# Kernel tuning notes

Measured on AMD Instinct MI355X. Metric: run time of the kernel, lower is better.

## Reference

```python
import jax, jax.numpy as jnp
import numpy as np

LN_EPS = 1e-5


def conv2d(x, w, b, stride, pad):
    # x: NCHW, w: OIHW
    y = jax.lax.conv_general_dilated(
        x, w, (stride, stride), [(pad, pad), (pad, pad)],
        dimension_numbers=("NCHW", "OIHW", "NCHW"))
    return y + b[None, :, None, None]


def gdn(x, gamma, beta):
    # y_c = x_c / sqrt(beta_c + sum_j gamma_cj * x_j^2)  (1x1 conv on x^2)
    norm = jnp.einsum("bchw,dc->bdhw", x * x, gamma) + beta[None, :, None, None]
    return x / jnp.sqrt(norm)


def layernorm(x, w, b):
    mu = jnp.mean(x, axis=-1, keepdims=True)
    var = jnp.var(x, axis=-1, keepdims=True)
    return (x - mu) / jnp.sqrt(var + LN_EPS) * w + b


def setup_inputs() -> dict:
    key = jax.random.key(0)
    ks = jax.random.split(key, 16)
    r = lambda i, shape: (jax.random.normal(ks[i], shape) * 0.02).astype(jnp.float32)
    N, M, K, D = 128, 192, 192, 128
    return {
        "x_p": jax.random.normal(ks[0], (4, 16, 3, 64, 64), jnp.float32),
        "y_g": jax.random.normal(ks[1], (64, K, 32), jnp.float32),
        "conv1_w": r(2, (N, 3, 5, 5)), "conv1_b": jnp.zeros((N,), jnp.float32),
        "gamma1": (0.1 * jnp.eye(N) + 1e-3).astype(jnp.float32), "beta1": jnp.ones((N,), jnp.float32),
        "conv2_w": r(3, (N, N, 5, 5)), "conv2_b": jnp.zeros((N,), jnp.float32),
        "gamma2": (0.1 * jnp.eye(N) + 1e-3).astype(jnp.float32), "beta2": jnp.ones((N,), jnp.float32),
        "conv3_w": r(4, (M, N, 3, 3)), "conv3_b": jnp.zeros((M,), jnp.float32),
        "ln_q_w": jnp.ones((M,), jnp.float32), "ln_q_b": jnp.zeros((M,), jnp.float32),
        "ln_kv_w": jnp.ones((K,), jnp.float32), "ln_kv_b": jnp.zeros((K,), jnp.float32),
        "ln_out_w": jnp.ones((M,), jnp.float32), "ln_out_b": jnp.zeros((M,), jnp.float32),
        "Wq": r(5, (D, M)), "Wk": r(6, (D, K)), "v_w": r(7, (1, D)),
        "Wv": r(8, (M, K)), "out_w": r(9, (M, M)), "out_b": jnp.zeros((M,), jnp.float32),
    }


def reference(x_p, y_g, conv1_w, conv1_b, gamma1, beta1, conv2_w, conv2_b,
              gamma2, beta2, conv3_w, conv3_b, ln_q_w, ln_q_b, ln_kv_w, ln_kv_b,
              ln_out_w, ln_out_b, Wq, Wk, v_w, Wv, out_w, out_b):
    B, P, C, Hp, Wp = x_p.shape
    x = x_p.reshape(B * P, C, Hp, Wp)
    # local encoder: conv s2 -> GDN -> conv s2 -> GDN -> conv s1 k3
    x = gdn(conv2d(x, conv1_w, conv1_b, 2, 2), gamma1, beta1)
    x = gdn(conv2d(x, conv2_w, conv2_b, 2, 2), gamma2, beta2)
    y_local = conv2d(x, conv3_w, conv3_b, 1, 1)          # (BP, M, h, w)
    BP, M, h, w = y_local.shape
    q = y_local.reshape(BP, M, h * w).transpose(0, 2, 1)  # (BP, Tq, M)
    kv = y_g.reshape(BP, y_g.shape[1], -1).transpose(0, 2, 1)  # (BP, Tk, K)
    q = layernorm(q, ln_q_w, ln_q_b)
    kv = layernorm(kv, ln_kv_w, ln_kv_b)
    # Bahdanau additive attention
    q_proj = jnp.einsum("bqm,dm->bqd", q, Wq)            # (BP, Tq, D)
    k_proj = jnp.einsum("bkc,dc->bkd", kv, Wk)           # (BP, Tk, D)
    energy = jnp.einsum("bqkd,d->bqk",
                        jnp.tanh(q_proj[:, :, None, :] + k_proj[:, None, :, :]),
                        v_w[0])                           # (BP, Tq, Tk)
    alpha = jax.nn.softmax(energy, axis=-1)
    v_proj = jnp.einsum("bkc,mc->bkm", kv, Wv)           # (BP, Tk, M)
    context = jnp.einsum("bqk,bkm->bqm", alpha, v_proj)
    context = jnp.einsum("bqm,nm->bqn", context, out_w) + out_b
    fused = layernorm(q + context, ln_out_w, ln_out_b)
    return fused.transpose(0, 2, 1).reshape(BP, M, h, w)
```

## Files before the change

kernel.cpp:

```cpp
#include <hip/hip_runtime.h>
#include <cstddef>
#include <cstdint>


typedef __bf16 bf16x8 __attribute__((ext_vector_type(8)));
typedef float floatx4 __attribute__((ext_vector_type(4)));
typedef unsigned short ushortT;
typedef unsigned short ushort8v __attribute__((ext_vector_type(8)));

#if __has_builtin(__builtin_amdgcn_exp2f)
#define EXP2F(x) __builtin_amdgcn_exp2f(x)
#else
#define EXP2F(x) exp2f(x)
#endif
#if __has_builtin(__builtin_amdgcn_rcpf)
#define RCPF(x) __builtin_amdgcn_rcpf(x)
#else
#define RCPF(x) (1.f / (x))
#endif

__device__ __forceinline__ ushortT f2bf(float f) {
  unsigned u = __builtin_bit_cast(unsigned, f);
  unsigned r = (u + 0x7FFFu + ((u >> 16) & 1u)) >> 16;
  return (ushortT)r;
}
__device__ __forceinline__ float bf2f(ushortT u) {
  return __builtin_bit_cast(float, ((unsigned)u) << 16);
}

static constexpr size_t OFF_X2BF = 4194304;
static constexpr size_t OFF_X3BF = 9437184;
static constexpr size_t OFF_QRAW = 10485760;
static constexpr size_t OFF_WBQ  = 21299200;
static constexpr size_t OFF_WBK  = 21311488;
static constexpr size_t OFF_WBV  = 21323776;
static constexpr size_t OFF_WBO  = 21342208;
static constexpr size_t OFF_WT2  = 26079232;
static constexpr size_t OFF_WT3  = 26284032;
static constexpr size_t OFF_WC1  = 26394624;
static constexpr size_t OFF_GB1  = 26406912;
static constexpr size_t OFF_GB2  = 26415104;
static constexpr size_t OFF_KP   = 0;
static constexpr size_t OFF_VT   = 262144;

__device__ __constant__ int d_TWI2[4][9] = {{ 0, 2, 4,10,12,14,20,22,24},
                                            { 1, 3,11,13,21,23, 0, 0, 0},
                                            { 5, 7, 9,15,17,19, 0, 0, 0},
                                            { 6, 8,16,18, 0, 0, 0, 0, 0}};
__device__ __constant__ int d_NT2[4] = {9, 6, 6, 4};

__device__ void dev_convw3(const float* w, ushortT* wt, int mode, int total,
                           int idx) {
  if (idx >= total) return;
  int j    = idx & 7;
  int om   = (idx >> 3) & 63;
  int kg   = (idx >> 9) & 3;
  int slab = idx >> 11;
  int mt, s, tap, T;
  if (mode == 0) {
    int ph;
    if (slab < 72) ph = 0; else if (slab < 120) ph = 1;
    else if (slab < 168) ph = 2; else ph = 3;
    const int st[4] = {0, 72, 120, 168};
    const int ns[4] = {36, 24, 24, 16};
    int rel = slab - st[ph];
    mt = rel / ns[ph]; s = rel % ns[ph];
    tap = d_TWI2[ph][s >> 2]; T = 25;
  } else {
    mt = slab / 36; s = slab % 36; tap = s >> 2; T = 9;
  }
  int cc = s & 3;
  int c  = cc * 32 + kg * 8 + j;
  int oc = mt * 64 + om;
  wt[idx] = f2bf(w[(size_t)(oc * 128 + c) * T + tap]);
}

__device__ void dev_convw1(const float* w, ushortT* wt, int idx) {
  if (idx >= 20480) return;
  int k    = idx & 31;
  int oc   = (idx >> 5) & 127;
  int slab = idx >> 12;
  int ph, i;
  if (slab < 2) { ph = 0; i = slab; } else { ph = slab - 1; i = 0; }
  int kg = k >> 3, jj = k & 7;
  int tidx = i * 8 + jj;
  float val = 0.f;
  if (kg < 3 && tidx < d_NT2[ph]) {
    int tap = d_TWI2[ph][tidx];
    val = w[(size_t)(oc * 3 + kg) * 25 + tap];
  }
  wt[idx] = f2bf(val);
}

__device__ void dev_wcast(const float* w, ushortT* wb, int total, float scale,
                          int idx) {
  if (idx < total) wb[idx] = f2bf(w[idx] * scale);
}

__global__ __launch_bounds__(256) void prep_kernel(
    const float* __restrict__ conv2_w, ushortT* __restrict__ wt2,
    const float* __restrict__ conv3_w, ushortT* __restrict__ wt3,
    const float* __restrict__ conv1_w, ushortT* __restrict__ wc1,
    const float* __restrict__ Wq, ushortT* __restrict__ wbq,
    const float* __restrict__ Wk, ushortT* __restrict__ wbk,
    const float* __restrict__ Wv, ushortT* __restrict__ wbv,
    const float* __restrict__ out_w, ushortT* __restrict__ wbo,
    const float* __restrict__ gamma1, ushortT* __restrict__ gb1,
    const float* __restrict__ gamma2, ushortT* __restrict__ gb2) {
  constexpr float C2LE = 2.88539008177792681f;
  int blk = blockIdx.x, tid = threadIdx.x;
  if (blk < 1600)      dev_convw3(conv2_w, wt2, 0, 409600, blk * 256 + tid);
  else if (blk < 2464) dev_convw3(conv3_w, wt3, 1, 221184, (blk - 1600) * 256 + tid);
  else if (blk < 2544) dev_convw1(conv1_w, wc1, (blk - 2464) * 256 + tid);
  else if (blk < 2640) dev_wcast(Wq, wbq, 24576, C2LE, (blk - 2544) * 256 + tid);
  else if (blk < 2736) dev_wcast(Wk, wbk, 24576, C2LE, (blk - 2640) * 256 + tid);
  else if (blk < 2880) dev_wcast(Wv, wbv, 36864, 1.f, (blk - 2736) * 256 + tid);
  else if (blk < 3024) dev_wcast(out_w, wbo, 36864, 1.f, (blk - 2880) * 256 + tid);
  else if (blk < 3088) dev_wcast(gamma1, gb1, 16384, 1.f, (blk - 3024) * 256 + tid);
  else                 dev_wcast(gamma2, gb2, 16384, 1.f, (blk - 3088) * 256 + tid);
}

__global__ __launch_bounds__(256, 2) void conv1_gdn_kernel(
    const float* __restrict__ x, const ushortT* __restrict__ wc1,
    const float* __restrict__ bias, const ushortT* __restrict__ gb1,
    const float* __restrict__ beta1, ushortT* __restrict__ outb) {
  int b  = blockIdx.x >> 3;
  int yg = blockIdx.x & 7;
  int y0 = yg * 4;

  int wave = threadIdx.x >> 6;
  int lane = threadIdx.x & 63;
  int ln15 = lane & 15;
  int kg   = lane >> 4;
  int tid  = threadIdx.x;

  __shared__ ushortT smem[28416];
  ushortT* simg = smem;
  ushortT* sA   = smem + 2816;

  for (int j = tid; j < 1408; j += 256) ((unsigned*)simg)[j] = 0u;
  __syncthreads();

  int ihBase = 2 * y0 - 2;
  const float* xb = x + (size_t)b * 3 * 4096;
  for (int j = tid; j < 576; j += 256) {
    int q = j & 15;
    int rr = j >> 4;
    int c = rr / 12, ihl = rr % 12;
    int ih = ihBase + ihl;
    if (ih >= 0 && ih < 64) {
      float4 v = *(const float4*)&xb[c * 4096 + ih * 64 + q * 4];
      int pr = ih & 1, u = ih >> 1;
      int lr = u - y0 + 1;
      int base0 = ((pr * 2 + 0) * 3 + c) * 216 + lr * 36;
      int base1 = ((pr * 2 + 1) * 3 + c) * 216 + lr * 36;
      simg[base0 + 2 * q + 1] = f2bf(v.x);
      simg[base1 + 2 * q + 1] = f2bf(v.y);
      simg[base0 + 2 * q + 2] = f2bf(v.z);
      simg[base1 + 2 * q + 2] = f2bf(v.w);
    }
  }
  for (int j = tid; j < 2560; j += 256) {
    int chunk = j & 3, row = j >> 2;
    uint4 v = *(const uint4*)&wc1[row * 32 + chunk * 8];
    *(uint4*)&sA[row * 40 + chunk * 8] = v;
  }
  __syncthreads();

  constexpr int TDR[4][9] = {{-1,-1,-1, 0, 0, 0, 1, 1, 1},
                             {-1,-1, 0, 0, 1, 1, 0, 0, 0},
                             {-1,-1,-1, 0, 0, 0, 0, 0, 0},
                             {-1,-1, 0, 0, 0, 0, 0, 0, 0}};
  constexpr int TDC[4][9] = {{-1, 0, 1,-1, 0, 1,-1, 0, 1},
                             {-1, 0,-1, 0,-1, 0, 0, 0, 0},
                             {-1, 0, 1,-1, 0, 1, 0, 0, 0},
                             {-1, 0,-1, 0, 0, 0, 0, 0, 0}};
  constexpr int NT[4]  = {9, 6, 6, 4};
  constexpr int NM[4]  = {2, 1, 1, 1};
  constexpr int SB[4]  = {0, 2, 3, 4};

  ushort8v Bf[2][5];
  #pragma unroll
  for (int ntl = 0; ntl < 2; ++ntl) {
    int ntg = wave * 2 + ntl;
    int yloc = ntg >> 1;
    int xx = (ntg & 1) * 16 + ln15;
    int lbase = (yloc + 1) * 36 + xx + 1 + kg * 216;
    #pragma unroll
    for (int ph = 0; ph < 4; ++ph) {
      int pbase = ph * 648 + lbase;
      #pragma unroll
      for (int i = 0; i < 2; ++i) {
        if (i < NM[ph]) {
          ushort8v bv;
          #pragma unroll
          for (int j = 0; j < 8; ++j) {
            int tidx = i * 8 + j;
            if (tidx >= NT[ph]) tidx = 0;
            int off = TDR[ph][tidx] * 36 + TDC[ph][tidx];
            bv[j] = simg[pbase + off];
          }
          Bf[ntl][SB[ph] + i] = bv;
        }
      }
    }
  }

  ushort4 xq[8][2];
  #pragma unroll
  for (int m = 0; m < 8; ++m) {
    bf16x8 Af[5];
    #pragma unroll
    for (int s = 0; s < 5; ++s)
      Af[s] = *(const bf16x8*)&sA[(s * 128 + m * 16 + ln15) * 40 + kg * 8];
    int oc0 = m * 16 + kg * 4;
    float4 bv = *(const float4*)&bias[oc0];
    #pragma unroll
    for (int ntl = 0; ntl < 2; ++ntl) {
      floatx4 acc = (floatx4)0.f;
      #pragma unroll
      for (int s = 0; s < 5; ++s)
        acc = __builtin_amdgcn_mfma_f32_16x16x32_bf16(
            Af[s], __builtin_bit_cast(bf16x8, Bf[ntl][s]), acc, 0, 0, 0);
      ushort4 o4 = {f2bf(acc[0] + bv.x), f2bf(acc[1] + bv.y),
                    f2bf(acc[2] + bv.z), f2bf(acc[3] + bv.w)};
      xq[m][ntl] = o4;
    }
  }
  __syncthreads();

  for (int j = tid; j < 2048; j += 256) {
    int row = j >> 4, ch = j & 15;
    *(uint4*)&smem[row * 136 + ch * 8] = *(const uint4*)&gb1[row * 128 + ch * 8];
  }
  __syncthreads();

  const int sxbase = 17408 + wave * 2176;
  #pragma unroll
  for (int q = 0; q < 2; ++q) {
    #pragma unroll
    for (int m = 0; m < 8; ++m) {
      ushort4 xv = xq[m][q];
      float f0 = bf2f(xv.x), f1 = bf2f(xv.y), f2 = bf2f(xv.z), f3 = bf2f(xv.w);
      ushort4 s4 = {f2bf(f0 * f0), f2bf(f1 * f1), f2bf(f2 * f2), f2bf(f3 * f3)};
      *(ushort4*)&smem[sxbase + ln15 * 136 + m * 16 + kg * 4] = s4;
    }
    int ntg = wave * 2 + q;
    int y = y0 + (ntg >> 1);
    int xx = (ntg & 1) * 16 + ln15;
    int ph = ((y & 1) << 1) | (xx & 1);
    size_t dstbase = (((size_t)b * 4 + ph) * 256 + (y >> 1) * 16 + (xx >> 1)) * 128;
    #pragma unroll
    for (int dt = 0; dt < 8; ++dt) {
      floatx4 acc = (floatx4)0.f;
      #pragma unroll
      for (int k0 = 0; k0 < 4; ++k0) {
        bf16x8 ga = *(const bf16x8*)&smem[(dt * 16 + ln15) * 136 + k0 * 32 + kg * 8];
        bf16x8 xbv = *(const bf16x8*)&smem[sxbase + ln15 * 136 + k0 * 32 + kg * 8];
        acc = __builtin_amdgcn_mfma_f32_16x16x32_bf16(ga, xbv, acc, 0, 0, 0);
      }
      int d0 = dt * 16 + kg * 4;
      float4 bt = *(const float4*)&beta1[d0];
      ushort4 xv = xq[dt][q];
      ushort4 o4;
      o4.x = f2bf(bf2f(xv.x) * rsqrtf(acc[0] + bt.x));
      o4.y = f2bf(bf2f(xv.y) * rsqrtf(acc[1] + bt.y));
      o4.z = f2bf(bf2f(xv.z) * rsqrtf(acc[2] + bt.z));
      o4.w = f2bf(bf2f(xv.w) * rsqrtf(acc[3] + bt.w));
      *(ushort4*)&outb[dstbase + d0] = o4;
    }
  }
}

__global__ __launch_bounds__(512, 2) void conv2_gdn_kernel(
    const ushortT* __restrict__ X, const ushortT* __restrict__ Wt,
    const float* __restrict__ bias, const ushortT* __restrict__ gb2,
    const float* __restrict__ beta2, ushortT* __restrict__ outb) {
  int b  = blockIdx.x >> 2;
  int rs = blockIdx.x & 3;
  int r0 = rs * 4;

  int tid  = threadIdx.x;
  int wave = tid >> 6;
  int lane = tid & 63;
  int ln15 = lane & 15;
  int kg   = lane >> 4;
  int wrow  = wave & 3;
  int whalf = wave >> 2;

  __shared__ ushortT smem[23392];
  ushortT* simg = smem;
  ushortT* sX2  = smem + 14688;

  floatx4 acc[4];
  #pragma unroll
  for (int m = 0; m < 4; ++m) acc[m] = (floatx4)0.f;

  constexpr int NS2[4]      = {36, 24, 24, 16};
  constexpr int PHSTART2[4] = {0, 72, 120, 168};
  constexpr int TDR_2[4][9] = {{-1,-1,-1, 0, 0, 0, 1, 1, 1},
                               {-1,-1, 0, 0, 1, 1, 0, 0, 0},
                               {-1,-1,-1, 0, 0, 0, 0, 0, 0},
                               {-1,-1, 0, 0, 0, 0, 0, 0, 0}};
  constexpr int TDC_2[4][9] = {{-1, 0, 1,-1, 0, 1,-1, 0, 1},
                               {-1, 0,-1, 0,-1, 0, 0, 0, 0},
                               {-1, 0, 1,-1, 0, 1, 0, 0, 0},
                               {-1, 0,-1, 0, 0, 0, 0, 0, 0}};

  const int aoff = kg * 512 + ln15 * 8;
  uint4 apf[8][4];

  #pragma unroll
  for (int ph = 0; ph < 4; ++ph) {
    const int NS = NS2[ph];
    const ushortT* wp0 = Wt + (size_t)(PHSTART2[ph] + whalf * NS) * 2048 + aoff;

    __syncthreads();
    const ushortT* Xb = X + (((size_t)b * 4 + ph) * 256) * 128;
    for (int idx = tid; idx < 1728; idx += 512) {
      int chunk = idx & 15;
      int pix = idx >> 4;
      int row = pix / 18, colm = pix - row * 18;
      int i = r0 - 1 + row, j = colm - 1;
      uint4 v = {0u, 0u, 0u, 0u};
      if (i >= 0 && i < 16 && j >= 0 && j < 16)
        v = *(const uint4*)(Xb + ((size_t)(i * 16 + j)) * 128 + chunk * 8);
      *(uint4*)&simg[(row * 18 + colm) * 136 + chunk * 8] = v;
    }
    #pragma unroll
    for (int jj = 0; jj < 8; ++jj) {
      #pragma unroll
      for (int m = 0; m < 4; ++m)
        apf[jj][m] = *(const uint4*)(wp0 + (size_t)jj * 2048 + m * 128);
    }
    __syncthreads();

    #pragma unroll
    for (int s0 = 0; s0 < NS; s0 += 8) {
      #pragma unroll
      for (int jj = 0; jj < 8; ++jj) {
        int s = s0 + jj;
        if (s < NS) {
          bf16x8 acur[4];
          #pragma unroll
          for (int m = 0; m < 4; ++m) acur[m] = __builtin_bit_cast(bf16x8, apf[jj][m]);
          int sp = s + 8;
          if (sp < NS) {
            #pragma unroll
            for (int m = 0; m < 4; ++m)
              apf[jj][m] = *(const uint4*)(wp0 + (size_t)sp * 2048 + m * 128);
          }
          int t  = s >> 2;
          int c0 = (s & 3) * 32;
          int dr = TDR_2[ph][t];
          int dc = TDC_2[ph][t];
          int lrow = wrow + dr + 1;
          int lcol = ln15 + dc + 1;
          bf16x8 bfr = *(const bf16x8*)&simg[(lrow * 18 + lcol) * 136 + c0 + kg * 8];
          #pragma unroll
          for (int m = 0; m < 4; ++m)
            acc[m] = __builtin_amdgcn_mfma_f32_16x16x32_bf16(acur[m], bfr, acc[m], 0, 0, 0);
        }
      }
    }
  }

  ushort4 xq2[4];
  #pragma unroll
  for (int m = 0; m < 4; ++m) {
    int mg = whalf * 64 + m * 16 + kg * 4;
    float4 bv = *(const float4*)&bias[mg];
    ushort4 o4 = {f2bf(acc[m][0] + bv.x), f2bf(acc[m][1] + bv.y),
                  f2bf(acc[m][2] + bv.z), f2bf(acc[m][3] + bv.w)};
    xq2[m] = o4;
    float f0 = bf2f(o4.x), f1 = bf2f(o4.y), f2 = bf2f(o4.z), f3 = bf2f(o4.w);
    ushort4 s4 = {f2bf(f0 * f0), f2bf(f1 * f1), f2bf(f2 * f2), f2bf(f3 * f3)};
    *(ushort4*)&sX2[(wrow * 16 + ln15) * 136 + mg] = s4;
  }
  __syncthreads();

  int p = (r0 + wrow) * 16 + ln15;
  size_t obase = ((size_t)b * 256 + p) * 128;
  #pragma unroll
  for (int dti = 0; dti < 4; ++dti) {
    int dt = whalf * 4 + dti;
    floatx4 nacc = (floatx4)0.f;
    #pragma unroll
    for (int k0 = 0; k0 < 4; ++k0) {
      bf16x8 ga = *(const bf16x8*)&gb2[(size_t)(dt * 16 + ln15) * 128 + k0 * 32 + kg * 8];
      bf16x8 xbv = *(const bf16x8*)&sX2[(wrow * 16 + ln15) * 136 + k0 * 32 + kg * 8];
      nacc = __builtin_amdgcn_mfma_f32_16x16x32_bf16(ga, xbv, nacc, 0, 0, 0);
    }
    int d0 = dt * 16 + kg * 4;
    float4 bt = *(const float4*)&beta2[d0];
    ushort4 xv = xq2[dti];
    ushort4 o4;
    o4.x = f2bf(bf2f(xv.x) * rsqrtf(nacc[0] + bt.x));
    o4.y = f2bf(bf2f(xv.y) * rsqrtf(nacc[1] + bt.y));
    o4.z = f2bf(bf2f(xv.z) * rsqrtf(nacc[2] + bt.z));
    o4.w = f2bf(bf2f(xv.w) * rsqrtf(nacc[3] + bt.w));
    *(ushort4*)&outb[obase + d0] = o4;
  }
}

__global__ __launch_bounds__(256, 2) void conv3_mfma_kernel(
    const ushortT* __restrict__ X,
    const ushortT* __restrict__ Wt,
    const float* __restrict__ bias,
    ushortT* __restrict__ outb) {
  constexpr int OC  = 192;
  constexpr int NMT = 3;

  int b   = blockIdx.x / (NMT * 4);
  int rem = blockIdx.x % (NMT * 4);
  int mt  = rem >> 2;
  int rs  = rem & 3;
  int r0  = rs * 4;

  int wave = threadIdx.x >> 6;
  int lane = threadIdx.x & 63;
  int ln15 = lane & 15;
  int kg   = lane >> 4;

  __shared__ ushortT simg[6 * 18 * 136];

  floatx4 acc[4];
  #pragma unroll
  for (int m = 0; m < 4; ++m) acc[m] = (floatx4)0.f;

  constexpr int TDR_3[9] = {-1,-1,-1, 0, 0, 0, 1, 1, 1};
  constexpr int TDC_3[9] = {-1, 0, 1,-1, 0, 1,-1, 0, 1};

  const int aoff = kg * 512 + ln15 * 8;
  uint4 apf[8][4];

  {
    const int NS = 36;
    const ushortT* wp0 = Wt + (size_t)(mt * 36) * 2048 + aoff;

    const ushortT* Xb = X + ((size_t)b * 256) * 128;
    for (int idx = threadIdx.x; idx < 1728; idx += 256) {
      int chunk = idx & 15;
      int pix = idx >> 4;
      int row = pix / 18, colm = pix - row * 18;
      int i = r0 - 1 + row, j = colm - 1;
      uint4 v = {0u, 0u, 0u, 0u};
      if (i >= 0 && i < 16 && j >= 0 && j < 16)
        v = *(const uint4*)(Xb + ((size_t)(i * 16 + j)) * 128 + chunk * 8);
      *(uint4*)&simg[(row * 18 + colm) * 136 + chunk * 8] = v;
    }
    #pragma unroll
    for (int jj = 0; jj < 8; ++jj) {
      #pragma unroll
      for (int m = 0; m < 4; ++m)
        apf[jj][m] = *(const uint4*)(wp0 + (size_t)jj * 2048 + m * 128);
    }
    __syncthreads();

    #pragma unroll
    for (int s0 = 0; s0 < NS; s0 += 8) {
      #pragma unroll
      for (int jj = 0; jj < 8; ++jj) {
        int s = s0 + jj;
        if (s < NS) {
          bf16x8 acur[4];
          #pragma unroll
          for (int m = 0; m < 4; ++m) acur[m] = __builtin_bit_cast(bf16x8, apf[jj][m]);
          int sp = s + 8;
          if (sp < NS) {
            #pragma unroll
            for (int m = 0; m < 4; ++m)
              apf[jj][m] = *(const uint4*)(wp0 + (size_t)sp * 2048 + m * 128);
          }
          int t  = s >> 2;
          int c0 = (s & 3) * 32;
          int lrow = wave + TDR_3[t] + 1;
          int lcol = ln15 + TDC_3[t] + 1;
          bf16x8 bfr = *(const bf16x8*)&simg[(lrow * 18 + lcol) * 136 + c0 + kg * 8];
          #pragma unroll
          for (int m = 0; m < 4; ++m)
            acc[m] = __builtin_amdgcn_mfma_f32_16x16x32_bf16(acur[m], bfr, acc[m], 0, 0, 0);
        }
      }
    }
  }

  #pragma unroll
  for (int m = 0; m < 4; ++m) {
    int mg = mt * 64 + m * 16 + kg * 4;
    float4 bv = *(const float4*)&bias[mg];
    int r = r0 + wave;
    int p = r * 16 + ln15;
    ushort4 o4 = {f2bf(acc[m][0] + bv.x), f2bf(acc[m][1] + bv.y),
                  f2bf(acc[m][2] + bv.z), f2bf(acc[m][3] + bv.w)};
    *(ushort4*)&outb[((size_t)b * 256 + p) * OC + mg] = o4;
  }
}

__global__ __launch_bounds__(256) void kv_prep_kernel(
    const float* __restrict__ yg, const float* __restrict__ ln_kv_w,
    const float* __restrict__ ln_kv_b, const ushortT* __restrict__ wbk,
    const ushortT* __restrict__ wbv, float* __restrict__ kp,
    ushortT* __restrict__ vT) {
  __shared__ float skvRaw[32 * 194];
  __shared__ ushortT skv[32 * 200];
  int b = blockIdx.x;
  int tid = threadIdx.x;
  int wave = tid >> 6, lane = tid & 63, ln15 = lane & 15, kg = lane >> 4;

  const float4* yg4 = (const float4*)(yg + (size_t)b * 6144);
  for (int j = tid; j < 1536; j += 256) {
    float4 v = yg4[j];
    int c = j >> 3;
    int t4 = (j & 7) * 4;
    skvRaw[(t4 + 0) * 194 + c] = v.x;
    skvRaw[(t4 + 1) * 194 + c] = v.y;
    skvRaw[(t4 + 2) * 194 + c] = v.z;
    skvRaw[(t4 + 3) * 194 + c] = v.w;
  }
  __syncthreads();
  for (int r = wave; r < 32; r += 4) {
    const float* src = skvRaw + r * 194;
    float v0 = src[lane], v1 = src[lane + 64], v2 = src[lane + 128];
    float s = v0 + v1 + v2;
    float s2 = v0 * v0 + v1 * v1 + v2 * v2;
    #pragma unroll
    for (int off = 32; off; off >>= 1) { s += __shfl_xor(s, off); s2 += __shfl_xor(s2, off); }
    float mean = s * (1.f / 192.f);
    float var = s2 * (1.f / 192.f) - mean * mean;
    float inv = rsqrtf(var + 1e-5f);
    skv[r * 200 + lane]       = f2bf((v0 - mean) * inv * ln_kv_w[lane]       + ln_kv_b[lane]);
    skv[r * 200 + lane + 64]  = f2bf((v1 - mean) * inv * ln_kv_w[lane + 64]  + ln_kv_b[lane + 64]);
    skv[r * 200 + lane + 128] = f2bf((v2 - mean) * inv * ln_kv_w[lane + 128] + ln_kv_b[lane + 128]);
  }
  __syncthreads();
  for (int ti = wave; ti < 40; ti += 4) {
    floatx4 acc = (floatx4)0.f;
    if (ti < 16) {
      int rt = ti >> 3, ct = ti & 7;
      #pragma unroll
      for (int k0 = 0; k0 < 192; k0 += 32) {
        bf16x8 afr = *(const bf16x8*)&skv[(rt * 16 + ln15) * 200 + k0 + kg * 8];
        bf16x8 bfr = *(const bf16x8*)&wbk[((size_t)(ct * 16 + ln15)) * 192 + k0 + kg * 8];
        acc = __builtin_amdgcn_mfma_f32_16x16x32_bf16(afr, bfr, acc, 0, 0, 0);
      }
      #pragma unroll
      for (int r = 0; r < 4; ++r)
        kp[((size_t)b * 32 + rt * 16 + kg * 4 + r) * 128 + ct * 16 + ln15] = acc[r];
    } else {
      int t2 = ti - 16;
      int rt = t2 / 12, ct = t2 % 12;
      #pragma unroll
      for (int k0 = 0; k0 < 192; k0 += 32) {
        bf16x8 afr = *(const bf16x8*)&skv[(rt * 16 + ln15) * 200 + k0 + kg * 8];
        bf16x8 bfr = *(const bf16x8*)&wbv[((size_t)(ct * 16 + ln15)) * 192 + k0 + kg * 8];
        acc = __builtin_amdgcn_mfma_f32_16x16x32_bf16(afr, bfr, acc, 0, 0, 0);
      }
      #pragma unroll
      for (int r = 0; r < 4; ++r)
        vT[((size_t)b * 192 + ct * 16 + ln15) * 32 + rt * 16 + kg * 4 + r] = f2bf(acc[r]);
    }
  }
}

__global__ __launch_bounds__(256, 4) void attn_kernel(
    const ushortT* __restrict__ qrawb, const float* __restrict__ ln_q_w,
    const float* __restrict__ ln_q_b, const float* __restrict__ kp,
    const ushortT* __restrict__ vT, const ushortT* __restrict__ wbq,
    const ushortT* __restrict__ wbo, const float* __restrict__ vw,
    const float* __restrict__ out_b, const float* __restrict__ ln_out_w,
    const float* __restrict__ ln_out_b, float* __restrict__ out) {
  __shared__ ushortT smem[17284];
  ushortT* sqln = smem;
  float*   skp  = (float*)(smem + 3200);
  float*   sqpF = (float*)(smem + 11648);
  float*   se   = (float*)(smem + 15872);
  float*   swm  = (float*)(smem + 17024);
  float*   sS0  = (float*)(smem + 17280);
  ushortT* sctx = smem;
  float*   sf   = (float*)(smem + 3200);

  int b  = blockIdx.x >> 4;
  int t0 = (blockIdx.x & 15) * 16;
  int tid  = threadIdx.x;
  int wave = tid >> 6;
  int lane = tid & 63;
  int ln15 = lane & 15;
  int kg   = lane >> 4;

  {
    const float4* kp4 = (const float4*)(kp + (size_t)b * 4096);
    for (int j = tid; j < 1024; j += 256) {
      int row = j >> 5, c4 = j & 31;
      *(float4*)&skp[row * 132 + c4 * 4] = kp4[j];
    }
  }
  float qreg[4][3];
  {
    float w0 = ln_q_w[lane], w1 = ln_q_w[lane + 64], w2 = ln_q_w[lane + 128];
    float b0 = ln_q_b[lane], b1 = ln_q_b[lane + 64], b2 = ln_q_b[lane + 128];
    #pragma unroll
    for (int i = 0; i < 4; ++i) {
      int r = wave + i * 4;
      const ushortT* xr = qrawb + ((size_t)(b * 256 + t0 + r)) * 192;
      float v0 = bf2f(xr[lane]), v1 = bf2f(xr[lane + 64]), v2 = bf2f(xr[lane + 128]);
      float s = v0 + v1 + v2;
      float s2 = v0 * v0 + v1 * v1 + v2 * v2;
      #pragma unroll
      for (int off = 32; off; off >>= 1) { s += __shfl_xor(s, off); s2 += __shfl_xor(s2, off); }
      float mean = s * (1.f / 192.f);
      float var = s2 * (1.f / 192.f) - mean * mean;
      float inv = rsqrtf(var + 1e-5f);
      float q0 = (v0 - mean) * inv * w0 + b0;
      float q1 = (v1 - mean) * inv * w1 + b1;
      float q2 = (v2 - mean) * inv * w2 + b2;
      qreg[i][0] = q0; qreg[i][1] = q1; qreg[i][2] = q2;
      sqln[r * 200 + lane]       = f2bf(q0);
      sqln[r * 200 + lane + 64]  = f2bf(q1);
      sqln[r * 200 + lane + 128] = f2bf(q2);
    }
  }
  if (tid < 128) swm[tid] = -2.f * vw[tid];
  if (tid >= 128 && tid < 192) {
    int l = tid - 128;
    float s = vw[l] + vw[l + 64];
    #pragma unroll
    for (int off = 32; off; off >>= 1) s += __shfl_xor(s, off);
    if (l == 0) *sS0 = s;
  }
  __syncthreads();

  for (int ti = wave; ti < 8; ti += 4) {
    floatx4 acc = (floatx4)0.f;
    #pragma unroll
    for (int k0 = 0; k0 < 192; k0 += 32) {
      bf16x8 afr = *(const bf16x8*)&sqln[ln15 * 200 + k0 + kg * 8];
      bf16x8 bfr = *(const bf16x8*)&wbq[((size_t)(ti * 16 + ln15)) * 192 + k0 + kg * 8];
      acc = __builtin_amdgcn_mfma_f32_16x16x32_bf16(afr, bfr, acc, 0, 0, 0);
    }
    #pragma unroll
    for (int r = 0; r < 4; ++r)
      sqpF[(kg * 4 + r) * 132 + ti * 16 + ln15] = acc[r];
  }
  __syncthreads();

  {
    float S0v = *sS0;
    int qq = tid >> 4, kc = tid & 15;
    const float4* w4 = (const float4*)swm;
    const float4* q4 = (const float4*)&sqpF[qq * 132];
    const float4* ka = (const float4*)&skp[kc * 132];
    const float4* kb = (const float4*)&skp[(kc + 16) * 132];
    float acc0 = S0v, acc1 = S0v;
    #pragma unroll 8
    for (int d4 = 0; d4 < 32; ++d4) {
      float4 qv = q4[d4], k0v = ka[d4], k1v = kb[d4], wv = w4[d4];
      acc0 += wv.x * RCPF(EXP2F(qv.x + k0v.x) + 1.f);
      acc0 += wv.y * RCPF(EXP2F(qv.y + k0v.y) + 1.f);
      acc0 += wv.z * RCPF(EXP2F(qv.z + k0v.z) + 1.f);
      acc0 += wv.w * RCPF(EXP2F(qv.w + k0v.w) + 1.f);
      acc1 += wv.x * RCPF(EXP2F(qv.x + k1v.x) + 1.f);
      acc1 += wv.y * RCPF(EXP2F(qv.y + k1v.y) + 1.f);
      acc1 += wv.z * RCPF(EXP2F(qv.z + k1v.z) + 1.f);
      acc1 += wv.w * RCPF(EXP2F(qv.w + k1v.w) + 1.f);
    }
    float mx = fmaxf(acc0, acc1);
    #pragma unroll
    for (int off = 8; off; off >>= 1) mx = fmaxf(mx, __shfl_xor(mx, off));
    float e0 = __expf(acc0 - mx), e1 = __expf(acc1 - mx);
    float s = e0 + e1;
    #pragma unroll
    for (int off = 8; off; off >>= 1) s += __shfl_xor(s, off);
    float inv = 1.f / s;
    se[qq * 36 + kc]      = e0 * inv;
    se[qq * 36 + kc + 16] = e1 * inv;
  }
  __syncthreads();

  {
    float4 a0 = *(const float4*)&se[ln15 * 36 + kg * 8];
    float4 a1 = *(const float4*)&se[ln15 * 36 + kg * 8 + 4];
    ushort8v au;
    au[0] = f2bf(a0.x); au[1] = f2bf(a0.y); au[2] = f2bf(a0.z); au[3] = f2bf(a0.w);
    au[4] = f2bf(a1.x); au[5] = f2bf(a1.y); au[6] = f2bf(a1.z); au[7] = f2bf(a1.w);
    for (int ti = wave; ti < 12; ti += 4) {
      bf16x8 bfr = *(const bf16x8*)&vT[((size_t)(b * 192 + ti * 16 + ln15)) * 32 + kg * 8];
      floatx4 acc = __builtin_amdgcn_mfma_f32_16x16x32_bf16(
          __builtin_bit_cast(bf16x8, au), bfr, (floatx4)0.f, 0, 0, 0);
      #pragma unroll
      for (int r = 0; r < 4; ++r)
        sctx[(kg * 4 + r) * 200 + ti * 16 + ln15] = f2bf(acc[r]);
    }
  }
  __syncthreads();

  for (int ti = wave; ti < 12; ti += 4) {
    floatx4 acc = (floatx4)0.f;
    #pragma unroll
    for (int k0 = 0; k0 < 192; k0 += 32) {
      bf16x8 afr = *(const bf16x8*)&sctx[ln15 * 200 + k0 + kg * 8];
      bf16x8 bfr = *(const bf16x8*)&wbo[((size_t)(ti * 16 + ln15)) * 192 + k0 + kg * 8];
      acc = __builtin_amdgcn_mfma_f32_16x16x32_bf16(afr, bfr, acc, 0, 0, 0);
    }
    float bv = out_b[ti * 16 + ln15];
    #pragma unroll
    for (int r = 0; r < 4; ++r)
      sf[(kg * 4 + r) * 193 + ti * 16 + ln15] = acc[r] + bv;
  }
  __syncthreads();

  #pragma unroll
  for (int i = 0; i < 4; ++i) {
    int rr = wave + i * 4;
    float v0 = sf[rr * 193 + lane]       + qreg[i][0];
    float v1 = sf[rr * 193 + lane + 64]  + qreg[i][1];
    float v2 = sf[rr * 193 + lane + 128] + qreg[i][2];
    float t_s = v0 + v1 + v2;
    float t_s2 = v0 * v0 + v1 * v1 + v2 * v2;
    #pragma unroll
    for (int off = 32; off; off >>= 1) { t_s += __shfl_xor(t_s, off); t_s2 += __shfl_xor(t_s2, off); }
    float m2 = t_s * (1.f / 192.f);
    float var2 = t_s2 * (1.f / 192.f) - m2 * m2;
    float inv2 = rsqrtf(var2 + 1e-5f);
    sf[rr * 193 + lane]       = (v0 - m2) * inv2 * ln_out_w[lane]       + ln_out_b[lane];
    sf[rr * 193 + lane + 64]  = (v1 - m2) * inv2 * ln_out_w[lane + 64]  + ln_out_b[lane + 64];
    sf[rr * 193 + lane + 128] = (v2 - m2) * inv2 * ln_out_w[lane + 128] + ln_out_b[lane + 128];
  }
  __syncthreads();

  for (int j = tid; j < 768; j += 256) {
    int m = j >> 2, t4 = j & 3;
    float4 o4;
    o4.x = sf[(t4 * 4 + 0) * 193 + m];
    o4.y = sf[(t4 * 4 + 1) * 193 + m];
    o4.z = sf[(t4 * 4 + 2) * 193 + m];
    o4.w = sf[(t4 * 4 + 3) * 193 + m];
    *(float4*)&out[((size_t)(b * 192 + m)) * 256 + t0 + t4 * 4] = o4;
  }
}

extern "C" void kernel_launch(void* const* d_in, const int* in_sizes, int n_in,
                              void* d_out, int out_size, void* d_ws, size_t ws_size,
                              hipStream_t stream) {
  (void)in_sizes; (void)n_in; (void)out_size; (void)ws_size;
  const float* x_p     = (const float*)d_in[0];
  const float* y_g     = (const float*)d_in[1];
  const float* conv1_w = (const float*)d_in[2];
  const float* conv1_b = (const float*)d_in[3];
  const float* gamma1  = (const float*)d_in[4];
  const float* beta1   = (const float*)d_in[5];
  const float* conv2_w = (const float*)d_in[6];
  const float* conv2_b = (const float*)d_in[7];
  const float* gamma2  = (const float*)d_in[8];
  const float* beta2   = (const float*)d_in[9];
  const float* conv3_w = (const float*)d_in[10];
  const float* conv3_b = (const float*)d_in[11];
  const float* ln_q_w  = (const float*)d_in[12];
  const float* ln_q_b  = (const float*)d_in[13];
  const float* ln_kv_w = (const float*)d_in[14];
  const float* ln_kv_b = (const float*)d_in[15];
  const float* ln_out_w= (const float*)d_in[16];
  const float* ln_out_b= (const float*)d_in[17];
  const float* Wq      = (const float*)d_in[18];
  const float* Wk      = (const float*)d_in[19];
  const float* v_w     = (const float*)d_in[20];
  const float* Wv      = (const float*)d_in[21];
  const float* out_w   = (const float*)d_in[22];
  const float* out_b   = (const float*)d_in[23];
  float* out = (float*)d_out;
  float* ws  = (float*)d_ws;

  ushortT* x2bf  = (ushortT*)(ws + OFF_X2BF);
  ushortT* x3bf  = (ushortT*)(ws + OFF_X3BF);
  ushortT* qrawb = (ushortT*)(ws + OFF_QRAW);
  ushortT* wbq   = (ushortT*)(ws + OFF_WBQ);
  ushortT* wbk   = (ushortT*)(ws + OFF_WBK);
  ushortT* wbv   = (ushortT*)(ws + OFF_WBV);
  ushortT* wbo   = (ushortT*)(ws + OFF_WBO);
  ushortT* wt2   = (ushortT*)(ws + OFF_WT2);
  ushortT* wt3   = (ushortT*)(ws + OFF_WT3);
  ushortT* wc1   = (ushortT*)(ws + OFF_WC1);
  ushortT* gb1   = (ushortT*)(ws + OFF_GB1);
  ushortT* gb2   = (ushortT*)(ws + OFF_GB2);
  float*   kp    = (float*)(ws + OFF_KP);
  ushortT* vTb   = (ushortT*)(ws + OFF_VT);

  prep_kernel<<<3152, 256, 0, stream>>>(conv2_w, wt2, conv3_w, wt3, conv1_w, wc1,
                                        Wq, wbq, Wk, wbk, Wv, wbv, out_w, wbo,
                                        gamma1, gb1, gamma2, gb2);
  kv_prep_kernel<<<64, 256, 0, stream>>>(y_g, ln_kv_w, ln_kv_b, wbk, wbv,
                                         kp, vTb);
  conv1_gdn_kernel<<<512, 256, 0, stream>>>(x_p, wc1, conv1_b, gb1, beta1, x2bf);
  conv2_gdn_kernel<<<256, 512, 0, stream>>>(x2bf, wt2, conv2_b, gb2, beta2, x3bf);
  conv3_mfma_kernel<<<768, 256, 0, stream>>>(x3bf, wt3, conv3_b, qrawb);
  attn_kernel<<<1024, 256, 0, stream>>>(qrawb, ln_q_w, ln_q_b, kp, vTb,
                                        wbq, wbo, v_w, out_b, ln_out_w,
                                        ln_out_b, out);
}
```

Measured before the change: 219.6 us.

## Stage conv2/conv3 weight slices through LDS with register double-buffering

Both the conv2+GDN and conv3 MFMA kernels stop prefetching a deep per-lane register array of weight fragments straight from global memory. Instead, threads cooperatively load weight slices into registers, store them into shared memory each step, prefetch the next slices, and read MFMA A-operands from LDS. This cuts register pressure and uses coalesced weight loads, at the cost of more LDS and two barriers per slice group. Occupancy may drop from the larger shared memory footprint.

```diff
diff --git a/kernel.cpp b/kernel.cpp
--- a/kernel.cpp
+++ b/kernel.cpp
@@ -288,8 +288,9 @@
   int wrow  = wave & 3;
   int whalf = wave >> 2;
 
-  __shared__ ushortT smem[23392];
+  __shared__ ushortT smem[31072];
   ushortT* simg = smem;
+  ushortT* sW   = smem + 14688;
   ushortT* sX2  = smem + 14688;
 
   floatx4 acc[4];
@@ -308,12 +309,11 @@
                                {-1, 0,-1, 0, 0, 0, 0, 0, 0}};
 
   const int aoff = kg * 512 + ln15 * 8;
-  uint4 apf[8][4];
 
   #pragma unroll
   for (int ph = 0; ph < 4; ++ph) {
     const int NS = NS2[ph];
-    const ushortT* wp0 = Wt + (size_t)(PHSTART2[ph] + whalf * NS) * 2048 + aoff;
+    const int P  = PHSTART2[ph];
 
     __syncthreads();
     const ushortT* Xb = X + (((size_t)b * 4 + ph) * 256) * 128;
@@ -327,43 +327,57 @@
         v = *(const uint4*)(Xb + ((size_t)(i * 16 + j)) * 128 + chunk * 8);
       *(uint4*)&simg[(row * 18 + colm) * 136 + chunk * 8] = v;
     }
-    #pragma unroll
-    for (int jj = 0; jj < 8; ++jj) {
-      #pragma unroll
-      for (int m = 0; m < 4; ++m)
-        apf[jj][m] = *(const uint4*)(wp0 + (size_t)jj * 2048 + m * 128);
-    }
-    __syncthreads();
-
-    #pragma unroll
-    for (int s0 = 0; s0 < NS; s0 += 8) {
-      #pragma unroll
-      for (int jj = 0; jj < 8; ++jj) {
-        int s = s0 + jj;
-        if (s < NS) {
-          bf16x8 acur[4];
-          #pragma unroll
-          for (int m = 0; m < 4; ++m) acur[m] = __builtin_bit_cast(bf16x8, apf[jj][m]);
-          int sp = s + 8;
-          if (sp < NS) {
-            #pragma unroll
-            for (int m = 0; m < 4; ++m)
-              apf[jj][m] = *(const uint4*)(wp0 + (size_t)sp * 2048 + m * 128);
-          }
-          int t  = s >> 2;
-          int c0 = (s & 3) * 32;
-          int dr = TDR_2[ph][t];
-          int dc = TDC_2[ph][t];
-          int lrow = wrow + dr + 1;
-          int lcol = ln15 + dc + 1;
-          bf16x8 bfr = *(const bf16x8*)&simg[(lrow * 18 + lcol) * 136 + c0 + kg * 8];
-          #pragma unroll
-          for (int m = 0; m < 4; ++m)
-            acc[m] = __builtin_amdgcn_mfma_f32_16x16x32_bf16(acur[m], bfr, acc[m], 0, 0, 0);
+
+    uint4 creg[4];
+    #pragma unroll
+    for (int j = 0; j < 4; ++j) {
+      int u = tid + j * 512;
+      int slot = u >> 8;
+      int off = (u & 255) * 8;
+      creg[j] = *(const uint4*)(Wt +
+          (size_t)(P + (slot >> 2) * NS + (slot & 3)) * 2048 + off);
+    }
+
+    for (int c0 = 0; c0 < NS; c0 += 4) {
+      __syncthreads();
+      #pragma unroll
+      for (int j = 0; j < 4; ++j) {
+        int u = tid + j * 512;
+        int slot = u >> 8;
+        int off = (u & 255) * 8;
+        *(uint4*)&sW[slot * 2048 + off] = creg[j];
+      }
+      if (c0 + 4 < NS) {
+        #pragma unroll
+        for (int j = 0; j < 4; ++j) {
+          int u = tid + j * 512;
+          int slot = u >> 8;
+          int off = (u & 255) * 8;
+          creg[j] = *(const uint4*)(Wt +
+              (size_t)(P + (slot >> 2) * NS + c0 + 4 + (slot & 3)) * 2048 + off);
         }
       }
-    }
-  }
+      __syncthreads();
+      #pragma unroll
+      for (int i = 0; i < 4; ++i) {
+        int s = c0 + i;
+        int t = s >> 2;
+        int cc = (s & 3) * 32;
+        int dr = TDR_2[ph][t];
+        int dc = TDC_2[ph][t];
+        bf16x8 bfr = *(const bf16x8*)&simg[((wrow + dr + 1) * 18 +
+                                            (ln15 + dc + 1)) * 136 + cc + kg * 8];
+        const ushortT* wsl = &sW[(whalf * 4 + i) * 2048 + aoff];
+        #pragma unroll
+        for (int m = 0; m < 4; ++m) {
+          bf16x8 af = *(const bf16x8*)&wsl[m * 128];
+          acc[m] = __builtin_amdgcn_mfma_f32_16x16x32_bf16(af, bfr, acc[m], 0, 0, 0);
+        }
+      }
+    }
+  }
+
+  __syncthreads();
 
   ushort4 xq2[4];
   #pragma unroll
@@ -417,12 +431,15 @@
   int rs  = rem & 3;
   int r0  = rs * 4;
 
-  int wave = threadIdx.x >> 6;
-  int lane = threadIdx.x & 63;
+  int tid  = threadIdx.x;
+  int wave = tid >> 6;
+  int lane = tid & 63;
   int ln15 = lane & 15;
   int kg   = lane >> 4;
 
-  __shared__ ushortT simg[6 * 18 * 136];
+  __shared__ ushortT smem[31072];
+  ushortT* simg = smem;
+  ushortT* sW   = smem + 14688;
 
   floatx4 acc[4];
   #pragma unroll
@@ -432,54 +449,52 @@
   constexpr int TDC_3[9] = {-1, 0, 1,-1, 0, 1,-1, 0, 1};
 
   const int aoff = kg * 512 + ln15 * 8;
-  uint4 apf[8][4];
-
-  {
-    const int NS = 36;
-    const ushortT* wp0 = Wt + (size_t)(mt * 36) * 2048 + aoff;
-
-    const ushortT* Xb = X + ((size_t)b * 256) * 128;
-    for (int idx = threadIdx.x; idx < 1728; idx += 256) {
-      int chunk = idx & 15;
-      int pix = idx >> 4;
-      int row = pix / 18, colm = pix - row * 18;
-      int i = r0 - 1 + row, j = colm - 1;
-      uint4 v = {0u, 0u, 0u, 0u};
-      if (i >= 0 && i < 16 && j >= 0 && j < 16)
-        v = *(const uint4*)(Xb + ((size_t)(i * 16 + j)) * 128 + chunk * 8);
-      *(uint4*)&simg[(row * 18 + colm) * 136 + chunk * 8] = v;
-    }
-    #pragma unroll
-    for (int jj = 0; jj < 8; ++jj) {
-      #pragma unroll
-      for (int m = 0; m < 4; ++m)
-        apf[jj][m] = *(const uint4*)(wp0 + (size_t)jj * 2048 + m * 128);
-    }
+
+  const ushortT* Xb = X + ((size_t)b * 256) * 128;
+  for (int idx = tid; idx < 1728; idx += 256) {
+    int chunk = idx & 15;
+    int pix = idx >> 4;
+    int row = pix / 18, colm = pix - row * 18;
+    int i = r0 - 1 + row, j = colm - 1;
+    uint4 v = {0u, 0u, 0u, 0u};
+    if (i >= 0 && i < 16 && j >= 0 && j < 16)
+      v = *(const uint4*)(Xb + ((size_t)(i * 16 + j)) * 128 + chunk * 8);
+    *(uint4*)&simg[(row * 18 + colm) * 136 + chunk * 8] = v;
+  }
+
+  uint4 creg[8];
+  #pragma unroll
+  for (int j = 0; j < 8; ++j)
+    creg[j] = *(const uint4*)(Wt + (size_t)(mt * 36 + j) * 2048 + tid * 8);
+
+  for (int c0 = 0; c0 < 36; c0 += 8) {
+    int cn = 36 - c0; if (cn > 8) cn = 8;
     __syncthreads();
-
-    #pragma unroll
-    for (int s0 = 0; s0 < NS; s0 += 8) {
-      #pragma unroll
-      for (int jj = 0; jj < 8; ++jj) {
-        int s = s0 + jj;
-        if (s < NS) {
-          bf16x8 acur[4];
-          #pragma unroll
-          for (int m = 0; m < 4; ++m) acur[m] = __builtin_bit_cast(bf16x8, apf[jj][m]);
-          int sp = s + 8;
-          if (sp < NS) {
-            #pragma unroll
-            for (int m = 0; m < 4; ++m)
-              apf[jj][m] = *(const uint4*)(wp0 + (size_t)sp * 2048 + m * 128);
-          }
-          int t  = s >> 2;
-          int c0 = (s & 3) * 32;
-          int lrow = wave + TDR_3[t] + 1;
-          int lcol = ln15 + TDC_3[t] + 1;
-          bf16x8 bfr = *(const bf16x8*)&simg[(lrow * 18 + lcol) * 136 + c0 + kg * 8];
-          #pragma unroll
-          for (int m = 0; m < 4; ++m)
-            acc[m] = __builtin_amdgcn_mfma_f32_16x16x32_bf16(acur[m], bfr, acc[m], 0, 0, 0);
+    #pragma unroll
+    for (int j = 0; j < 8; ++j)
+      if (j < cn) *(uint4*)&sW[j * 2048 + tid * 8] = creg[j];
+    if (c0 + 8 < 36) {
+      int nn = 36 - (c0 + 8); if (nn > 8) nn = 8;
+      #pragma unroll
+      for (int j = 0; j < 8; ++j)
+        if (j < nn)
+          creg[j] = *(const uint4*)(Wt + (size_t)(mt * 36 + c0 + 8 + j) * 2048 + tid * 8);
+    }
+    __syncthreads();
+    #pragma unroll
+    for (int i = 0; i < 8; ++i) {
+      if (i < cn) {
+        int s = c0 + i;
+        int t = s >> 2;
+        int cc = (s & 3) * 32;
+        int lrow = wave + TDR_3[t] + 1;
+        int lcol = ln15 + TDC_3[t] + 1;
+        bf16x8 bfr = *(const bf16x8*)&simg[(lrow * 18 + lcol) * 136 + cc + kg * 8];
+        const ushortT* wsl = &sW[i * 2048 + aoff];
+        #pragma unroll
+        for (int m = 0; m < 4; ++m) {
+          bf16x8 af = *(const bf16x8*)&wsl[m * 128];
+          acc[m] = __builtin_amdgcn_mfma_f32_16x16x32_bf16(af, bfr, acc[m], 0, 0, 0);
         }
       }
     }
```

Result: slower. 273.2 us (+24.4%).
